# Kernel tuning notes

Hardware: AMD Instinct MI355X
Metric: run time of the kernel (lower is better)

## Reference

```python
import jax, jax.numpy as jnp
import numpy as np

NUM_LEVELS = 4
RADIUS = 4
DISP_SCALE = 64.0  # disparity magnitude range for synthetic inputs


def build_corr_pyramid(full_corr, num_levels=NUM_LEVELS):
    """full_corr: (B, Wr, H, Wl). Avg-pool (k=2, s=2, ceil_mode) along Wr per level."""
    pyr = [full_corr]
    cur = full_corr
    for _ in range(1, num_levels):
        B, Wr, H, Wl = cur.shape
        n2 = (Wr // 2) * 2
        pooled = cur[:, :n2].reshape(B, Wr // 2, 2, H, Wl).mean(axis=2)
        if Wr % 2 == 1:
            # ceil_mode: trailing window clipped to a single element
            pooled = jnp.concatenate([pooled, cur[:, -1:]], axis=1)
        pyr.append(pooled)
        cur = pooled
    return pyr


def sample_corr_pyramid_bilinear(pyr, disp, radius=RADIUS):
    """pyr[l]: (B, Wr_l, H, Wl); disp: (B,1,H,Wl).
    Sample 1D-bilinearly along Wr at index (i_left - disp)/2^l + off, off in [-r, r].
    Returns (B, K*L, H, Wl), K = 2r+1.
    """
    B, _, H, Wl = pyr[0].shape
    K = 2 * radius + 1
    base = jnp.arange(Wl, dtype=disp.dtype).reshape(1, 1, 1, Wl)
    offs = jnp.arange(-radius, radius + 1, dtype=disp.dtype).reshape(1, K, 1, 1)
    bi = jnp.arange(B).reshape(B, 1, 1, 1)
    hi = jnp.arange(H).reshape(1, 1, H, 1)
    wi = jnp.arange(Wl).reshape(1, 1, 1, Wl)
    outs = []
    for l, corr in enumerate(pyr):
        Wr_l = corr.shape[1]
        idx_c = (base - disp) / (2.0 ** l)          # (B,1,H,Wl)
        idx = jnp.clip(idx_c + offs, 0.0, Wr_l - 1)  # (B,K,H,Wl)
        idx0 = jnp.clip(jnp.floor(idx), 0.0, Wr_l - 1)
        idx1 = jnp.clip(idx0 + 1.0, 0.0, Wr_l - 1)
        w1 = idx - idx0
        i0 = idx0.astype(jnp.int32)
        i1 = idx1.astype(jnp.int32)
        # fused gather+interp: no (B,K,Wr_l,H,Wl) expansion
        v0 = corr[bi, i0, hi, wi]  # (B,K,H,Wl)
        v1 = corr[bi, i1, hi, wi]
        outs.append((1.0 - w1) * v0 + w1 * v1)
    return jnp.concatenate(outs, axis=1)  # (B, K*L, H, Wl)


def setup_inputs() -> dict:
    key = jax.random.key(0)
    k1, k2 = jax.random.split(key)
    B, Wr, H, Wl = 4, 320, 240, 320
    full_corr = jax.random.normal(k1, (B, Wr, H, Wl), dtype=jnp.float32)
    disp = jax.random.uniform(k2, (B, 1, H, Wl), dtype=jnp.float32) * DISP_SCALE
    return {"full_corr": full_corr, "disp": disp}


def reference(full_corr, disp):
    pyr = build_corr_pyramid(full_corr, NUM_LEVELS)
    return sample_corr_pyramid_bilinear(pyr, disp, RADIUS)
```

## Files before the change

kernel.cpp:

```cpp
#include <hip/hip_runtime.h>

#define NB 4
#define WR 320
#define NH 240
#define WL 320
#define NLEV 4
#define NK 9
#define TW 16
#define NTILES (WL / TW)
#define HH 4
#define BAND_LO 96
#define BAND_HI 56
#define ROWS (BAND_LO + BAND_HI)
#define NGROUPS (ROWS / 4)
#define RSTRIDE ((size_t)NH * WL)
#define NXCD 8

typedef const __attribute__((address_space(1))) void* gas_t;
typedef __attribute__((address_space(3))) void* las_t;

__device__ __forceinline__ void gld_lds16(const float* g, float* l) {
  __builtin_amdgcn_global_load_lds((gas_t)g, (las_t)l, 16, 0, 0);
}

template <int L>
__device__ __forceinline__ void sample_level(const float* __restrict__ lds,
                                             int hh, int c, int row_lo,
                                             float idx_c,
                                             float* __restrict__ outp) {
  const int Wrl = WR >> L;
  const int Wm1 = Wrl - 1;
  const float sc = 1.0f / (float)(1 << L);
  const float fidx = idx_c * sc;

  auto pooled = [&](int j) -> float {
    const int s = (j << L) - row_lo;
    const int o = (s << 6) + (hh << 4) + c;
    float v = lds[o];
#pragma unroll
    for (int t = 1; t < (1 << L); ++t) v += lds[o + (t << 6)];
    return v * sc;
  };

  float idk = fminf(fmaxf(fidx - 4.0f, 0.0f), (float)Wm1);
  int j = (int)idk;
  float vA = pooled(j);
  float vB = pooled(min(j + 1, Wm1));

#pragma unroll
  for (int k = 0; k < NK; ++k) {
    const float idx = fminf(fmaxf(fidx + (float)(k - 4), 0.0f), (float)Wm1);
    const int i0 = (int)idx;
    if (i0 != j) {
      vA = vB;
      vB = pooled(min(i0 + 1, Wm1));
      j = i0;
    }
    const float w = idx - (float)i0;
    outp[(size_t)k * RSTRIDE] = fmaf(w, vB - vA, vA);
  }
}

extern "C" __global__ __launch_bounds__(256, 4) void corr_sample_kernel(
    const float* __restrict__ corr, const float* __restrict__ disp,
    float* __restrict__ out) {
  __shared__ float lds0[ROWS * HH * TW];

  const int bid0 = blockIdx.x;
  const int bid = (bid0 & (NXCD - 1)) * (NB * (NH / HH) * NTILES / NXCD) +
                  (bid0 >> 3);
  const int tile = bid % NTILES;
  const int hp = (bid / NTILES) % (NH / HH);
  const int b = bid / (NTILES * (NH / HH));
  const int w0 = tile * TW;
  const int h0 = hp * HH;
  const int row_lo = w0 - BAND_LO;

  const int tid = (int)threadIdx.x;
  const int lane = tid & 63;
  const int wv = tid >> 6;

  {
    const int ds = lane >> 4;
    const int sh = (lane >> 2) & 3;
    const int c4 = (lane & 3) << 2;
    for (int g = wv; g < NGROUPS; g += 4) {
      const int r0 = row_lo + 4 * g;
      if (r0 < 0 || r0 >= WR) continue;
      const float* src =
          corr + ((size_t)(b * WR + r0 + ds) * NH + (h0 + sh)) * WL + w0 + c4;
      gld_lds16(src, &lds0[g * (4 * HH * TW)]);
    }
  }

  const int hh = lane >> 4;
  const int c = lane & 15;
  const float dsp = disp[((size_t)b * NH + (h0 + hh)) * WL + w0 + c];

  asm volatile("s_waitcnt vmcnt(0)" ::: "memory");
  __syncthreads();

  const float idx_c = (float)(w0 + c) - dsp;
  float* outp = out + ((size_t)(b * (NLEV * NK) + wv * NK) * NH + (h0 + hh)) * WL +
                w0 + c;

  switch (wv) {
    case 0: sample_level<0>(lds0, hh, c, row_lo, idx_c, outp); break;
    case 1: sample_level<1>(lds0, hh, c, row_lo, idx_c, outp); break;
    case 2: sample_level<2>(lds0, hh, c, row_lo, idx_c, outp); break;
    default: sample_level<3>(lds0, hh, c, row_lo, idx_c, outp); break;
  }
}

extern "C" void kernel_launch(void* const* d_in, const int* in_sizes, int n_in,
                              void* d_out, int out_size, void* d_ws,
                              size_t ws_size, hipStream_t stream) {
  const float* corr = (const float*)d_in[0];
  const float* disp = (const float*)d_in[1];
  float* out = (float*)d_out;
  const int grid = NB * (NH / HH) * NTILES;
  corr_sample_kernel<<<grid, 256, 0, stream>>>(corr, disp, out);
}
```

Before: 42.12 us.

## Double-buffer LDS staging across row pairs with persistent per-block loop

Each block now handles 20 rows of H in 10 steps of two rows, double-buffering the correlation band and disparity in LDS so global loads for step q+2 overlap compute on step q. Each wave issues its share of the band loads and waits with counted vmcnt and barriers. Each wave still owns one pyramid level, now splitting the nine taps across lane halves. The grid shrinks from 4800 to 960 blocks, giving fewer blocks with more latency hiding but less parallelism and more barrier synchronisation.

After: 45.42 us. 1.08x slower.

```diff
diff --git a/kernel.cpp b/kernel.cpp
--- a/kernel.cpp
+++ b/kernel.cpp
@@ -4,111 +4,138 @@
 #define WR 320
 #define NH 240
 #define WL 320
-#define NLEV 4
 #define NK 9
 #define TW 16
-#define NTILES (WL / TW)
-#define HH 4
-#define BAND_LO 96
-#define BAND_HI 56
-#define ROWS (BAND_LO + BAND_HI)
-#define NGROUPS (ROWS / 4)
+#define NTILES 20
+#define NS 10
+#define HP 12
+#define SLOTS 152
+#define NI 19
+#define BANDF (SLOTS * 2 * TW)
+#define BUFSZ (BANDF + 64)
 #define RSTRIDE ((size_t)NH * WL)
+#define NBLK (NB * NTILES * HP)
 #define NXCD 8
 
 typedef const __attribute__((address_space(1))) void* gas_t;
 typedef __attribute__((address_space(3))) void* las_t;
 
-__device__ __forceinline__ void gld_lds16(const float* g, float* l) {
+__device__ __forceinline__ void gld16(const float* g, float* l) {
   __builtin_amdgcn_global_load_lds((gas_t)g, (las_t)l, 16, 0, 0);
+}
+__device__ __forceinline__ void gld4(const float* g, float* l) {
+  __builtin_amdgcn_global_load_lds((gas_t)g, (las_t)l, 4, 0, 0);
 }
 
 template <int L>
-__device__ __forceinline__ void sample_level(const float* __restrict__ lds,
-                                             int hh, int c, int row_lo,
-                                             float idx_c,
-                                             float* __restrict__ outp) {
-  const int Wrl = WR >> L;
-  const int Wm1 = Wrl - 1;
+__device__ __forceinline__ float pooledf(const float* p, int j, int sbase,
+                                         int hc) {
+  const int a = ((j << L) + sbase) * 32 + hc;
+  float v = p[a];
+#pragma unroll
+  for (int t = 1; t < (1 << L); ++t) v += p[a + t * 32];
+  return v;
+}
+
+template <int L>
+__device__ __forceinline__ void run_level(const float* __restrict__ corr,
+                                          const float* __restrict__ disp,
+                                          float* __restrict__ out, float* lds,
+                                          int b, int h0, int w0, int lane) {
+  const int dsr = lane >> 3;
+  const int sh = (lane >> 2) & 1;
+  const int c4 = (lane & 3) << 2;
+  const int kq2 = lane >> 5;
+  const int hh = (lane >> 4) & 1;
+  const int c = lane & 15;
+  const int hc = hh * 16 + c;
+  const int sbase = 96 - w0;
   const float sc = 1.0f / (float)(1 << L);
-  const float fidx = idx_c * sc;
+  const int Wm1 = (WR >> L) - 1;
+  const size_t cb = (size_t)b * WR * RSTRIDE;
 
-  auto pooled = [&](int j) -> float {
-    const int s = (j << L) - row_lo;
-    const int o = (s << 6) + (hh << 4) + c;
-    float v = lds[o];
+  auto stage = [&](int qs) {
+    float* bb = lds + (qs & 1) * BUFSZ;
 #pragma unroll
-    for (int t = 1; t < (1 << L); ++t) v += lds[o + (t << 6)];
-    return v * sc;
+    for (int i = L; i < NI; i += 4) {
+      int rr = w0 - 96 + 8 * i + dsr;
+      rr = min(max(rr, 0), WR - 1);
+      const float* src =
+          corr + cb + ((size_t)rr * NH + (h0 + 2 * qs + sh)) * WL + w0 + c4;
+      gld16(src, bb + i * 256);
+    }
+    if (L == 3) {
+      const float* dsrc =
+          disp + ((size_t)b * NH + (h0 + 2 * qs + ((lane >> 4) & 1))) * WL +
+          w0 + (lane & 15);
+      gld4(dsrc, bb + BANDF);
+    }
   };
 
-  float idk = fminf(fmaxf(fidx - 4.0f, 0.0f), (float)Wm1);
-  int j = (int)idk;
-  float vA = pooled(j);
-  float vB = pooled(min(j + 1, Wm1));
+  stage(0);
+  stage(1);
 
 #pragma unroll
-  for (int k = 0; k < NK; ++k) {
-    const float idx = fminf(fmaxf(fidx + (float)(k - 4), 0.0f), (float)Wm1);
-    const int i0 = (int)idx;
-    if (i0 != j) {
-      vA = vB;
-      vB = pooled(min(i0 + 1, Wm1));
-      j = i0;
+  for (int q = 0; q < NS; ++q) {
+    if (q == 0 || q == NS - 1)
+      asm volatile("s_waitcnt vmcnt(5)" ::: "memory");
+    else
+      asm volatile("s_waitcnt vmcnt(10)" ::: "memory");
+    __builtin_amdgcn_s_barrier();
+    __builtin_amdgcn_sched_barrier(0);
+
+    const float* bp = lds + (q & 1) * BUFSZ;
+    const float dsp = bp[BANDF + hc];
+    const float fidx = ((float)(w0 + c) - dsp) * sc;
+    const int hq = h0 + 2 * q + hh;
+
+#pragma unroll
+    for (int m = 0; m < 5; ++m) {
+      const int kraw = kq2 + 2 * m;
+      const int k = min(kraw, 8);
+      const float idx =
+          fminf(fmaxf(fidx + (float)(k - 4), 0.0f), (float)Wm1);
+      const int i0 = (int)idx;
+      const int i1 = min(i0 + 1, Wm1);
+      const float w = idx - (float)i0;
+      const float v0 = pooledf<L>(bp, i0, sbase, hc);
+      const float v1 = pooledf<L>(bp, i1, sbase, hc);
+      if (kraw < NK) {
+        out[((size_t)(b * (4 * NK) + L * NK + k) * NH + hq) * WL + w0 + c] =
+            sc * fmaf(w, v1 - v0, v0);
+      }
     }
-    const float w = idx - (float)i0;
-    outp[(size_t)k * RSTRIDE] = fmaf(w, vB - vA, vA);
+
+    asm volatile("" ::: "memory");
+    __builtin_amdgcn_s_barrier();
+    asm volatile("" ::: "memory");
+    if (q + 2 < NS) stage(q + 2);
+    asm volatile("" ::: "memory");
   }
 }
 
 extern "C" __global__ __launch_bounds__(256, 4) void corr_sample_kernel(
     const float* __restrict__ corr, const float* __restrict__ disp,
     float* __restrict__ out) {
-  __shared__ float lds0[ROWS * HH * TW];
+  __shared__ float lds0[2 * BUFSZ];
 
-  const int bid0 = blockIdx.x;
-  const int bid = (bid0 & (NXCD - 1)) * (NB * (NH / HH) * NTILES / NXCD) +
-                  (bid0 >> 3);
+  const int bid = ((int)blockIdx.x & (NXCD - 1)) * (NBLK / NXCD) +
+                  ((int)blockIdx.x >> 3);
   const int tile = bid % NTILES;
-  const int hp = (bid / NTILES) % (NH / HH);
-  const int b = bid / (NTILES * (NH / HH));
+  const int rest = bid / NTILES;
+  const int hp = rest % HP;
+  const int b = rest / HP;
   const int w0 = tile * TW;
-  const int h0 = hp * HH;
-  const int row_lo = w0 - BAND_LO;
+  const int h0 = hp * (2 * NS);
 
-  const int tid = (int)threadIdx.x;
-  const int lane = tid & 63;
-  const int wv = tid >> 6;
-
-  {
-    const int ds = lane >> 4;
-    const int sh = (lane >> 2) & 3;
-    const int c4 = (lane & 3) << 2;
-    for (int g = wv; g < NGROUPS; g += 4) {
-      const int r0 = row_lo + 4 * g;
-      if (r0 < 0 || r0 >= WR) continue;
-      const float* src =
-          corr + ((size_t)(b * WR + r0 + ds) * NH + (h0 + sh)) * WL + w0 + c4;
-      gld_lds16(src, &lds0[g * (4 * HH * TW)]);
-    }
-  }
-
-  const int hh = lane >> 4;
-  const int c = lane & 15;
-  const float dsp = disp[((size_t)b * NH + (h0 + hh)) * WL + w0 + c];
-
-  asm volatile("s_waitcnt vmcnt(0)" ::: "memory");
-  __syncthreads();
-
-  const float idx_c = (float)(w0 + c) - dsp;
-  float* outp = out + ((size_t)(b * (NLEV * NK) + wv * NK) * NH + (h0 + hh)) * WL +
-                w0 + c;
+  const int lane = (int)threadIdx.x & 63;
+  const int wv = (int)threadIdx.x >> 6;
 
   switch (wv) {
-    case 0: sample_level<0>(lds0, hh, c, row_lo, idx_c, outp); break;
-    case 1: sample_level<1>(lds0, hh, c, row_lo, idx_c, outp); break;
-    case 2: sample_level<2>(lds0, hh, c, row_lo, idx_c, outp); break;
-    default: sample_level<3>(lds0, hh, c, row_lo, idx_c, outp); break;
+    case 0: run_level<0>(corr, disp, out, lds0, b, h0, w0, lane); break;
+    case 1: run_level<1>(corr, disp, out, lds0, b, h0, w0, lane); break;
+    case 2: run_level<2>(corr, disp, out, lds0, b, h0, w0, lane); break;
+    default: run_level<3>(corr, disp, out, lds0, b, h0, w0, lane); break;
   }
 }
 
@@ -118,6 +145,5 @@
   const float* corr = (const float*)d_in[0];
   const float* disp = (const float*)d_in[1];
   float* out = (float*)d_out;
-  const int grid = NB * (NH / HH) * NTILES;
-  corr_sample_kernel<<<grid, 256, 0, stream>>>(corr, disp, out);
+  corr_sample_kernel<<<NBLK, 256, 0, stream>>>(corr, disp, out);
 }
```
